# Kernel tuning notes

Measured on AMD Instinct MI355X. Metric: run time of the kernel, lower is better.

## Reference

```python
import jax, jax.numpy as jnp
import numpy as np

# --- static configuration (mirrors PMETorchPME(alpha=1.0, mesh=1.0), interpolation_nodes=6) ---
ALPHA = 1.0            # Gaussian smearing sigma of CoulombPotential
MESH_SPACING = 1.0
BOX_L = 120.0
NS = (120, 120, 120)   # ceil(BOX_L / MESH_SPACING) per axis; static for jit
ORDER = 6              # interpolation nodes (6-point stencil per axis)
N_ATOMS = 100000
PI = np.pi


def _interp_weights(x):
    # x: (N,3) offsets in [-0.5, 0.5) relative to the midpoint of the 6-point stencil.
    # Lagrange interpolation on nodes t_j = j - 2.5, j = 0..5 (even-order, midpoint-centered).
    t = np.arange(ORDER) - (ORDER - 1) / 2.0                 # (6,) node positions
    diff = x[..., None] - jnp.asarray(t, x.dtype)            # (N,3,6)
    ws = []
    for j in range(ORDER):
        idx = [k for k in range(ORDER) if k != j]
        denom = float(np.prod([t[j] - t[k] for k in idx]))
        ws.append(jnp.prod(diff[..., idx], axis=-1) / denom)
    return jnp.stack(ws, axis=-1)                            # (N,3,6)


def _stencil(coords, box):
    # Map positions to mesh units, build per-particle 6x6x6 stencil weights + flat mesh indices.
    frac = coords @ jnp.linalg.inv(box)                      # fractional coordinates
    pos = frac * jnp.asarray(NS, coords.dtype)               # (N,3) in mesh units
    i0 = jnp.floor(pos)
    x = pos - (i0 + 0.5)                                     # offset from stencil midpoint
    w = _interp_weights(x)                                   # (N,3,6)
    offs = jnp.arange(ORDER, dtype=jnp.int32) - (ORDER // 2 - 1)   # [-2..3]
    ns_i = jnp.asarray(NS, jnp.int32)
    g = (i0.astype(jnp.int32)[..., None] + offs) % ns_i[None, :, None]  # (N,3,6) periodic
    W = w[:, 0, :, None, None] * w[:, 1, None, :, None] * w[:, 2, None, None, :]   # (N,6,6,6)
    flat = (g[:, 0, :, None, None] * NS[1] + g[:, 1, None, :, None]) * NS[2] + g[:, 2, None, None, :]
    n = coords.shape[0]
    return W.reshape(n, -1), flat.reshape(n, -1)             # (N,216) each


def _kspace_kernel(box, dtype):
    # G(k) = 4*pi * exp(-sigma^2 k^2 / 2) / k^2, zero at k=0 (CoulombPotential.lr_from_k_sq)
    inv_cell = jnp.linalg.inv(box)
    m0 = jnp.fft.fftfreq(NS[0]) * NS[0]
    m1 = jnp.fft.fftfreq(NS[1]) * NS[1]
    m2 = jnp.fft.rfftfreq(NS[2]) * NS[2]
    m = jnp.stack(jnp.meshgrid(m0, m1, m2, indexing="ij"), axis=-1).astype(dtype)
    k = 2.0 * PI * jnp.einsum("xyzm,nm->xyzn", m, inv_cell)  # k = 2*pi * inv(cell) @ m
    k_sq = jnp.sum(k * k, axis=-1)
    safe = jnp.where(k_sq > 0, k_sq, 1.0)
    return jnp.where(k_sq > 0, 4.0 * PI * jnp.exp(-0.5 * ALPHA * ALPHA * k_sq) / safe, 0.0)


def setup_inputs() -> dict:
    key = jax.random.key(0)
    k1, k2 = jax.random.split(key)
    coords = jax.random.uniform(k1, (N_ATOMS, 3), dtype=jnp.float32) * BOX_L
    box = (BOX_L * jnp.eye(3, dtype=jnp.float32))
    charges = jax.random.normal(k2, (N_ATOMS, 1), dtype=jnp.float32)
    return {"coords": coords, "box": box, "charges": charges}


def reference(coords, box, charges):
    q = charges[:, 0]                                        # (N,)
    W, flat = _stencil(coords, box)                          # (N,216)
    ntot = NS[0] * NS[1] * NS[2]
    # charge spreading (scatter-add)
    mesh = jnp.zeros((ntot,), coords.dtype).at[flat.reshape(-1)].add((W * q[:, None]).reshape(-1))
    mesh = mesh.reshape(NS)
    # FFT convolution with the reciprocal-space Coulomb kernel
    G = _kspace_kernel(box, coords.dtype)
    pot_mesh = jnp.fft.irfftn(jnp.fft.rfftn(mesh, norm="backward") * G, s=NS, norm="forward")
    # gather back to particles
    pot = jnp.sum(pot_mesh.reshape(-1)[flat] * W, axis=-1)   # (N,)
    volume = jnp.abs(jnp.linalg.det(box))
    pot = pot / volume
    pot = pot - q * (np.sqrt(2.0 / PI) / ALPHA)              # remove self-contribution
    pot = pot - 2.0 * (PI * ALPHA * ALPHA) * jnp.sum(q) / volume  # charge-neutral background
    pot = pot / 2.0
    return jnp.sum(q * pot)                                  # energy = sum(charges * potentials)
```

## Files before the change

kernel.cpp:

```cpp
#include <hip/hip_runtime.h>
#include <math.h>

#define NMESH 120
#define NKZ 61
#define ALPHA_C 1.0

#define TILE 12
#define NTPD 10
#define NTILE 1000
#define FP 17
#define FPCELLS (FP*FP*FP)
#define FPSTRIDE 4928
#define CAP 256

#define CHUNK 128
#define WXA_OFF 0
#define WYA_OFF (CHUNK*17)
#define WZA_OFF (2*CHUNK*17)
#define LXS_OFF (2*CHUNK*17 + CHUNK*20)
#define SMEMF   (LXS_OFF + CHUNK)

#define YCH 12
#define XCH 4
#define YROW 137

#define NSLOT 64
#define SLOTSTRIDE 8
#define W120C (-0.052359877559829887f)

#define EK_OFF      0
#define Q_OFF       4096
#define Q2_OFF      8192
#define BUF_OFF     115264
#define C1_OFF      19827264
#define C2_OFF      115264
#define COUNTS_OFF  C1_OFF
#define SORTED_OFF  (C1_OFF + 4096)

__device__ inline void inv3(const float* b, float* ib) {
    float a00=b[0],a01=b[1],a02=b[2],a10=b[3],a11=b[4],a12=b[5],a20=b[6],a21=b[7],a22=b[8];
    float c00 =  a11*a22 - a12*a21;
    float c01 = -(a10*a22 - a12*a20);
    float c02 =  a10*a21 - a11*a20;
    float c10 = -(a01*a22 - a02*a21);
    float c11 =  a00*a22 - a02*a20;
    float c12 = -(a00*a21 - a01*a20);
    float c20 =  a01*a12 - a02*a11;
    float c21 = -(a00*a12 - a02*a10);
    float c22 =  a00*a11 - a01*a10;
    float det = a00*c00 + a01*c01 + a02*c02;
    float inv = 1.0f/det;
    ib[0]=c00*inv; ib[1]=c10*inv; ib[2]=c20*inv;
    ib[3]=c01*inv; ib[4]=c11*inv; ib[5]=c21*inv;
    ib[6]=c02*inv; ib[7]=c12*inv; ib[8]=c22*inv;
}

__device__ inline void atom_pos(const float* __restrict__ box, float c0, float c1, float c2,
                                float* p) {
    float ib[9]; inv3(box, ib);
    #pragma unroll
    for (int d=0; d<3; ++d)
        p[d] = (c0*ib[0+d] + c1*ib[3+d] + c2*ib[6+d]) * 120.0f;
}

__device__ inline int wrap120(int i) { return ((i % 120) + 120) % 120; }

__device__ inline void lag6(float x, float* w) {
    float df[6];
    #pragma unroll
    for (int k=0;k<6;++k) df[k] = x - ((float)k - 2.5f);
    w[0] = df[1]*df[2]*df[3]*df[4]*df[5] * (-1.0f/120.0f);
    w[1] = df[0]*df[2]*df[3]*df[4]*df[5] * ( 1.0f/24.0f);
    w[2] = df[0]*df[1]*df[3]*df[4]*df[5] * (-1.0f/12.0f);
    w[3] = df[0]*df[1]*df[2]*df[4]*df[5] * ( 1.0f/12.0f);
    w[4] = df[0]*df[1]*df[2]*df[3]*df[5] * (-1.0f/24.0f);
    w[5] = df[0]*df[1]*df[2]*df[3]*df[4] * ( 1.0f/120.0f);
}

__device__ inline int halo_pairs(int c, int* t, int* l) {
    int r = c % 12, ti = c / 12, n = 0;
    t[n] = ti;          l[n] = r + 2;  n++;
    if (r < 3)  { t[n] = (ti+9)%10; l[n] = r + 14; n++; }
    if (r >= 10){ t[n] = (ti+1)%10; l[n] = r - 10; n++; }
    return n;
}

__device__ inline void dft8(const float2* xin, float2* Y) {
    const float S = 0.70710678118654752f;
    float2 a=xin[0], b=xin[2], c=xin[4], d=xin[6];
    float s02r=a.x+c.x, s02i=a.y+c.y, d02r=a.x-c.x, d02i=a.y-c.y;
    float s13r=b.x+d.x, s13i=b.y+d.y, d13r=b.x-d.x, d13i=b.y-d.y;
    float2 E0 = make_float2(s02r+s13r, s02i+s13i);
    float2 E1 = make_float2(d02r+d13i, d02i-d13r);
    float2 E2 = make_float2(s02r-s13r, s02i-s13i);
    float2 E3 = make_float2(d02r-d13i, d02i+d13r);
    a=xin[1]; b=xin[3]; c=xin[5]; d=xin[7];
    s02r=a.x+c.x; s02i=a.y+c.y; d02r=a.x-c.x; d02i=a.y-c.y;
    s13r=b.x+d.x; s13i=b.y+d.y; d13r=b.x-d.x; d13i=b.y-d.y;
    float2 O0 = make_float2(s02r+s13r, s02i+s13i);
    float2 O1 = make_float2(d02r+d13i, d02i-d13r);
    float2 O2 = make_float2(s02r-s13r, s02i-s13i);
    float2 O3 = make_float2(d02r-d13i, d02i+d13r);
    float t1r = S*(O1.x + O1.y), t1i = S*(O1.y - O1.x);
    float t2r = O2.y,            t2i = -O2.x;
    float t3r = S*(O3.y - O3.x), t3i = -S*(O3.x + O3.y);
    Y[0] = make_float2(E0.x + O0.x, E0.y + O0.y);
    Y[4] = make_float2(E0.x - O0.x, E0.y - O0.y);
    Y[1] = make_float2(E1.x + t1r,  E1.y + t1i);
    Y[5] = make_float2(E1.x - t1r,  E1.y - t1i);
    Y[2] = make_float2(E2.x + t2r,  E2.y + t2i);
    Y[6] = make_float2(E2.x - t2r,  E2.y - t2i);
    Y[3] = make_float2(E3.x + t3r,  E3.y + t3i);
    Y[7] = make_float2(E3.x - t3r,  E3.y - t3i);
}

__global__ void init_kernel(int* __restrict__ counts, double* __restrict__ slots) {
    int idx = threadIdx.x;
    for (int i = idx; i < 3*NSLOT*SLOTSTRIDE; i += 1024) slots[i] = 0.0;
    for (int i = idx; i < NTILE; i += 1024) counts[i] = 0;
}

__global__ void scatter_q_kernel(const float* __restrict__ coords,
                                 const float* __restrict__ box,
                                 const float* __restrict__ charges,
                                 int* __restrict__ counts,
                                 float4* __restrict__ sorted,
                                 double* __restrict__ qslots,
                                 double* __restrict__ q2slots, int n) {
    int i = blockIdx.x*blockDim.x + threadIdx.x;
    float v = 0.f, v2 = 0.f;
    if (i < n) {
        float p[3]; atom_pos(box, coords[3*i], coords[3*i+1], coords[3*i+2], p);
        float q = charges[i];
        v = q; v2 = q*q;
        int t[3];
        #pragma unroll
        for (int d=0; d<3; ++d) t[d] = wrap120((int)floorf(p[d])) / TILE;
        int tile = (t[0]*NTPD + t[1])*NTPD + t[2];
        int idx = atomicAdd(&counts[tile], 1);
        if (idx < CAP) sorted[tile*CAP + idx] = make_float4(p[0], p[1], p[2], q);
    }
    #pragma unroll
    for (int o=32;o>0;o>>=1) { v += __shfl_down(v,o,64); v2 += __shfl_down(v2,o,64); }
    __shared__ float s1[4], s2[4];
    int lane = threadIdx.x & 63, w = threadIdx.x >> 6;
    if (lane==0) { s1[w]=v; s2[w]=v2; }
    __syncthreads();
    if (threadIdx.x==0) {
        for (int j=1;j<4;j++) { v += s1[j]; v2 += s2[j]; }
        int slot = (blockIdx.x & (NSLOT-1)) * SLOTSTRIDE;
        atomicAdd(&qslots[slot],  (double)v);
        atomicAdd(&q2slots[slot], (double)v2);
    }
}

__global__ void __launch_bounds__(320)
spread_tile_kernel(const float4* __restrict__ sorted,
                   const int* __restrict__ counts,
                   float* __restrict__ buf) {
    int tile = blockIdx.x;
    int tx = tile / (NTPD*NTPD);
    int rem = tile - tx*NTPD*NTPD;
    int ty = rem / NTPD;
    int tz = rem - ty*NTPD;
    int bx = tx*TILE, by = ty*TILE, bz = tz*TILE;

    __shared__ float smem[SMEMF];
    int* lxs = (int*)&smem[LXS_OFF];

    int tid = threadIdx.x;
    int A = tid / 17, B = tid - A*17;
    int Ac = (A > 16) ? 16 : A;
    int wv = tid >> 6, lane = tid & 63;
    int Alo = (wv*64)/17;
    int Ahi = (wv*64+63)/17; if (Ahi > 16) Ahi = 16;

    float acc[17];
    #pragma unroll
    for (int k=0;k<17;++k) acc[k] = 0.f;

    int cntT = min(counts[tile], CAP);
    const float4* src = sorted + (size_t)tile*CAP;

    for (int start = 0; start < cntT; start += CHUNK) {
        int jn = cntT - start; if (jn > CHUNK) jn = CHUNK;
        __syncthreads();
        if (tid < jn) {
            float4 s = src[start + tid];
            float fx = floorf(s.x), fy = floorf(s.y), fz = floorf(s.z);
            float wx[6]; lag6(s.x - (fx + 0.5f), wx);
            float wy[6]; lag6(s.y - (fy + 0.5f), wy);
            float wz[6]; lag6(s.z - (fz + 0.5f), wz);
            int lx = wrap120((int)fx) - bx;
            int ly = wrap120((int)fy) - by;
            int lz = wrap120((int)fz) - bz;
            #pragma unroll
            for (int k=0;k<17;++k) { smem[WXA_OFF + tid*17 + k] = 0.f;
                                     smem[WYA_OFF + tid*17 + k] = 0.f; }
            float4* wzp = (float4*)&smem[WZA_OFF + tid*20];
            float4 zz4 = make_float4(0.f,0.f,0.f,0.f);
            #pragma unroll
            for (int k=0;k<5;++k) wzp[k] = zz4;
            #pragma unroll
            for (int k=0;k<6;++k) {
                smem[WXA_OFF + tid*17 + lx + k] = wx[k];
                smem[WYA_OFF + tid*17 + ly + k] = wy[k];
                smem[WZA_OFF + tid*20 + lz + k] = wz[k]*s.w;
            }
            lxs[tid] = lx;
        }
        __syncthreads();
        int l0 = lxs[lane], l1 = lxs[64+lane];
        bool g0 = (lane < jn)    && (l0 <= Ahi) && (l0 + 5 >= Alo);
        bool g1 = (64+lane < jn) && (l1 <= Ahi) && (l1 + 5 >= Alo);
        unsigned long long m0 = __ballot(g0);
        unsigned long long m1 = __ballot(g1);
        auto body = [&](int j) {
            float wx_ = smem[WXA_OFF + j*17 + Ac];
            float wy_ = smem[WYA_OFF + j*17 + B];
            float w2 = wx_ * wy_;
            const float4* zp = (const float4*)&smem[WZA_OFF + j*20];
            float4 z0 = zp[0], z1 = zp[1], z2 = zp[2], z3 = zp[3];
            float z16 = smem[WZA_OFF + j*20 + 16];
            acc[0] = fmaf(w2,z0.x,acc[0]);  acc[1] = fmaf(w2,z0.y,acc[1]);
            acc[2] = fmaf(w2,z0.z,acc[2]);  acc[3] = fmaf(w2,z0.w,acc[3]);
            acc[4] = fmaf(w2,z1.x,acc[4]);  acc[5] = fmaf(w2,z1.y,acc[5]);
            acc[6] = fmaf(w2,z1.z,acc[6]);  acc[7] = fmaf(w2,z1.w,acc[7]);
            acc[8] = fmaf(w2,z2.x,acc[8]);  acc[9] = fmaf(w2,z2.y,acc[9]);
            acc[10]= fmaf(w2,z2.z,acc[10]); acc[11]= fmaf(w2,z2.w,acc[11]);
            acc[12]= fmaf(w2,z3.x,acc[12]); acc[13]= fmaf(w2,z3.y,acc[13]);
            acc[14]= fmaf(w2,z3.z,acc[14]); acc[15]= fmaf(w2,z3.w,acc[15]);
            acc[16]= fmaf(w2,z16, acc[16]);
        };
        while (m0) { int j = __builtin_ctzll(m0); m0 &= m0-1ull; body(j); }
        while (m1) { int j = 64 + __builtin_ctzll(m1); m1 &= m1-1ull; body(j); }
    }
    __syncthreads();
    if (tid < 289) {
        #pragma unroll
        for (int k=0;k<17;++k) smem[tid*17 + k] = acc[k];
    }
    __syncthreads();
    for (int i = tid; i < FPCELLS; i += 320)
        buf[(size_t)tile * FPSTRIDE + i] = smem[i];
}

#define DFT15_BODY(Yp, kfreq, RE, IM)                                        \
    float w1r = tw[kfreq].x, w1i = tw[kfreq].y;                              \
    float w2r = w1r*w1r - w1i*w1i, w2i = 2.f*w1r*w1i;                        \
    float w3r = w2r*w1r - w2i*w1i, w3i = w2r*w1i + w2i*w1r;                  \
    float ar=1.f, ai=0.f, br=w1r, bi=w1i, cr=w2r, ci=w2i;                    \
    float r0_=0.f,i0_=0.f,r1_=0.f,i1_=0.f,r2_=0.f,i2_=0.f;                   \
    _Pragma("unroll")                                                        \
    for (int s_=0;s_<5;++s_) {                                               \
        float2 ya = (Yp)[3*s_], yb = (Yp)[3*s_+1], yc = (Yp)[3*s_+2];        \
        r0_ = fmaf(ya.x, ar, fmaf(-ya.y, ai, r0_));                          \
        i0_ = fmaf(ya.x, ai, fmaf( ya.y, ar, i0_));                          \
        r1_ = fmaf(yb.x, br, fmaf(-yb.y, bi, r1_));                          \
        i1_ = fmaf(yb.x, bi, fmaf( yb.y, br, i1_));                          \
        r2_ = fmaf(yc.x, cr, fmaf(-yc.y, ci, r2_));                          \
        i2_ = fmaf(yc.x, ci, fmaf( yc.y, cr, i2_));                          \
        float n_;                                                            \
        n_ = ar*w3r - ai*w3i; ai = ar*w3i + ai*w3r; ar = n_;                 \
        n_ = br*w3r - bi*w3i; bi = br*w3i + bi*w3r; br = n_;                 \
        n_ = cr*w3r - ci*w3i; ci = cr*w3i + ci*w3r; cr = n_;                 \
    }                                                                        \
    float RE = (r0_+r1_)+r2_, IM = (i0_+i1_)+i2_;

#define TWIDDLE_INIT()                                                       \
    __shared__ float2 tw[120];                                               \
    for (int k_ = threadIdx.x; k_ < 120; k_ += blockDim.x) {                 \
        float s_, c_; __sincosf(W120C * (float)k_, &s_, &c_);                \
        tw[k_] = make_float2(c_, s_);                                        \
    }

__global__ void __launch_bounds__(256)
fft_z_kernel(const float* __restrict__ buf,
             float2* __restrict__ C1) {
    int x  = blockIdx.x / 10;
    int y0 = (blockIdx.x - x*10) * YCH;
    __shared__ float  lin[YCH][121];
    __shared__ float2 Ys[YCH][YROW];
    TWIDDLE_INIT()

    int txA[2], lxA[2];
    int nx = halo_pairs(x, txA, lxA);

    for (int i = threadIdx.x; i < YCH*120; i += 256) {
        int yl = i / 120, z = i - yl*120;
        int tyA[2], lyA[2]; int ny = halo_pairs(y0 + yl, tyA, lyA);
        int tzA[2], lzA[2]; int nz = halo_pairs(z, tzA, lzA);
        float s = 0.f;
        for (int ii=0; ii<nx; ++ii)
            for (int jj=0; jj<ny; ++jj)
                for (int kk=0; kk<nz; ++kk) {
                    int tile = (txA[ii]*NTPD + tyA[jj])*NTPD + tzA[kk];
                    int cell = (lxA[ii]*FP + lyA[jj])*FP + lzA[kk];
                    s += buf[(size_t)tile*FPSTRIDE + cell];
                }
        lin[yl][z] = s;
    }
    __syncthreads();
    for (int t = threadIdx.x; t < YCH*15; t += 256) {
        int yl = t / 15, j = t - (t/15)*15;
        float2 xin[8], Yo[8];
        #pragma unroll
        for (int m=0;m<8;++m) xin[m] = make_float2(lin[yl][15*m+j], 0.f);
        dft8(xin, Yo);
        #pragma unroll
        for (int r=0;r<8;++r) Ys[yl][r*17+j] = Yo[r];
    }
    __syncthreads();
    for (int o = threadIdx.x; o < YCH*NKZ; o += 256) {
        int kz = o / YCH, yl = o - (o/YCH)*YCH;
        const float2* Yp = &Ys[yl][(kz&7)*17];
        DFT15_BODY(Yp, kz, re, im)
        C1[(x*NKZ + kz)*120 + y0 + yl] = make_float2(re, im);
    }
}

__global__ void __launch_bounds__(256)
fft_y_kernel(const float2* __restrict__ C1,
             float2* __restrict__ C2) {
    int xc = blockIdx.x / NKZ;
    int kz = blockIdx.x - xc*NKZ;
    int x0 = xc * XCH;
    __shared__ float2 lin[XCH][121];
    __shared__ float2 Ys[XCH][YROW];
    TWIDDLE_INIT()
    for (int i = threadIdx.x; i < XCH*120; i += 256) {
        int xo = i / 120, y = i - (i/120)*120;
        lin[xo][y] = C1[((x0+xo)*NKZ + kz)*120 + y];
    }
    __syncthreads();
    for (int t = threadIdx.x; t < XCH*15; t += 256) {
        int xo = t / 15, j = t - (t/15)*15;
        float2 xin[8], Yo[8];
        #pragma unroll
        for (int m=0;m<8;++m) xin[m] = lin[xo][15*m+j];
        dft8(xin, Yo);
        #pragma unroll
        for (int r=0;r<8;++r) Ys[xo][r*17+j] = Yo[r];
    }
    __syncthreads();
    for (int o = threadIdx.x; o < XCH*120; o += 256) {
        int ky = o >> 2, xo = o & 3;
        const float2* Yp = &Ys[xo][(ky&7)*17];
        DFT15_BODY(Yp, ky, re, im)
        C2[(kz*120 + ky)*120 + x0 + xo] = make_float2(re, im);
    }
}

__global__ void __launch_bounds__(256)
fft_x_energy_kernel(const float2* __restrict__ C2,
                    const float* __restrict__ box,
                    double* __restrict__ ekslots) {
    int kyc = blockIdx.x / NKZ;
    int kz  = blockIdx.x - kyc*NKZ;
    int ky0 = kyc * XCH;
    __shared__ float2 lin[XCH][121];
    __shared__ float2 Ys[XCH][YROW];
    TWIDDLE_INIT()
    const float2* src = C2 + (kz*120 + ky0)*120;
    for (int i = threadIdx.x; i < XCH*120; i += 256) {
        int kyo = i / 120, xx = i - (i/120)*120;
        lin[kyo][xx] = src[i];
    }
    __syncthreads();
    for (int t = threadIdx.x; t < XCH*15; t += 256) {
        int kyo = t / 15, j = t - (t/15)*15;
        float2 xin[8], Yo[8];
        #pragma unroll
        for (int m=0;m<8;++m) xin[m] = lin[kyo][15*m+j];
        dft8(xin, Yo);
        #pragma unroll
        for (int r=0;r<8;++r) Ys[kyo][r*17+j] = Yo[r];
    }
    __syncthreads();
    float ib[9]; inv3(box, ib);
    const float TWOPI = 6.283185307179586f;
    float wzf = (kz==0 || kz==60) ? 1.0f : 2.0f;
    float contrib = 0.f;
    for (int o = threadIdx.x; o < XCH*120; o += 256) {
        int kyo = o / 120, kx = o - (o/120)*120;
        int ky = ky0 + kyo;
        const float2* Yp = &Ys[kyo][(kx&7)*17];
        DFT15_BODY(Yp, kx, re, im)
        if (!(kx==0 && ky==0 && kz==0)) {
            float mx = (kx < 60) ? (float)kx : (float)(kx - 120);
            float my = (ky < 60) ? (float)ky : (float)(ky - 120);
            float mz = (float)kz;
            float k0 = TWOPI*(mx*ib[0] + my*ib[1] + mz*ib[2]);
            float k1 = TWOPI*(mx*ib[3] + my*ib[4] + mz*ib[5]);
            float k2 = TWOPI*(mx*ib[6] + my*ib[7] + mz*ib[8]);
            float ksq = k0*k0 + k1*k1 + k2*k2;
            float G = 12.566370614359172f * __expf(-0.5f*(float)(ALPHA_C*ALPHA_C)*ksq) / ksq;
            contrib += wzf * G * (re*re + im*im);
        }
    }
    #pragma unroll
    for (int o=32;o>0;o>>=1) contrib += __shfl_down(contrib,o,64);
    __shared__ float sm[4];
    int lane = threadIdx.x & 63, w = threadIdx.x >> 6;
    if (lane==0) sm[w] = contrib;
    __syncthreads();
    if (threadIdx.x==0)
        atomicAdd(&ekslots[(blockIdx.x & (NSLOT-1)) * SLOTSTRIDE],
                  (double)(sm[0]+sm[1]+sm[2]+sm[3]));
}

__global__ void finalize_kernel(const double* __restrict__ ekslots,
                                const double* __restrict__ qslots,
                                const double* __restrict__ q2slots,
                                const float* __restrict__ box,
                                float* __restrict__ out) {
    int lane = threadIdx.x;
    double ek  = ekslots[lane*SLOTSTRIDE];
    double sq  = qslots [lane*SLOTSTRIDE];
    double sq2 = q2slots[lane*SLOTSTRIDE];
    #pragma unroll
    for (int o=32;o>0;o>>=1) {
        ek  += __shfl_down(ek,  o, 64);
        sq  += __shfl_down(sq,  o, 64);
        sq2 += __shfl_down(sq2, o, 64);
    }
    if (lane == 0) {
        double a00=box[0],a01=box[1],a02=box[2],a10=box[3],a11=box[4],a12=box[5],a20=box[6],a21=box[7],a22=box[8];
        double det = a00*(a11*a22-a12*a21) - a01*(a10*a22-a12*a20) + a02*(a10*a21-a11*a20);
        double vol = fabs(det);
        double E = ek/(2.0*vol)
                 - 0.5*sqrt(2.0/M_PI)/ALPHA_C * sq2
                 - M_PI*ALPHA_C*ALPHA_C * sq*sq / vol;
        out[0] = (float)E;
    }
}

extern "C" void kernel_launch(void* const* d_in, const int* in_sizes, int n_in,
                              void* d_out, int out_size, void* d_ws, size_t ws_size,
                              hipStream_t stream) {
    const float* coords  = (const float*)d_in[0];
    const float* box     = (const float*)d_in[1];
    const float* charges = (const float*)d_in[2];
    int n = in_sizes[0] / 3;

    char* ws = (char*)d_ws;
    double* ekslots = (double*)(ws + EK_OFF);
    double* qslots  = (double*)(ws + Q_OFF);
    double* q2slots = (double*)(ws + Q2_OFF);
    float*  buf     = (float*) (ws + BUF_OFF);
    float2* C1      = (float2*)(ws + C1_OFF);
    float2* C2      = (float2*)(ws + C2_OFF);
    int* counts     = (int*)(ws + COUNTS_OFF);
    float4* sorted  = (float4*)(ws + SORTED_OFF);

    int gA = (n + 255)/256;
    init_kernel<<<1, 1024, 0, stream>>>(counts, ekslots);
    scatter_q_kernel<<<gA, 256, 0, stream>>>(coords, box, charges, counts, sorted, qslots, q2slots, n);
    spread_tile_kernel<<<NTILE, 320, 0, stream>>>(sorted, counts, buf);
    fft_z_kernel<<<120*10, 256, 0, stream>>>(buf, C1);
    fft_y_kernel<<<30*NKZ, 256, 0, stream>>>(C1, C2);
    fft_x_energy_kernel<<<NKZ*30, 256, 0, stream>>>(C2, box, ekslots);
    finalize_kernel<<<1, 64, 0, stream>>>(ekslots, qslots, q2slots, box, (float*)d_out);
}
```

Before: 147.7 us.

## Restructure tile spreading into 128-thread blocks with packed 2-wide FMA accumulation

The spread kernel now runs 128 threads per tile. Each owner thread accumulates a column of 17 z-cells times 4 y-cells using packed float2 FMAs and float4 weight loads, instead of 289 threads each holding one (x,y) column. The footprint layout is padded to a stride of 20 in z so both the shared-memory and global writes can be float4-vectorised. The init kernel is replaced by two hipMemsetAsync calls. This aims to cut shared-memory loads per FMA, raise occupancy and speed up stores, but it adds larger per-thread register state, a bigger buffer, and a more complex skip scheme for the second wave.

```diff
diff --git a/kernel.cpp b/kernel.cpp
--- a/kernel.cpp
+++ b/kernel.cpp
@@ -9,16 +9,16 @@
 #define NTPD 10
 #define NTILE 1000
 #define FP 17
-#define FPCELLS (FP*FP*FP)
-#define FPSTRIDE 4928
+#define ZPAD 20
+#define FPSTRIDE 5792
 #define CAP 256
 
 #define CHUNK 128
 #define WXA_OFF 0
-#define WYA_OFF (CHUNK*17)
-#define WZA_OFF (2*CHUNK*17)
-#define LXS_OFF (2*CHUNK*17 + CHUNK*20)
-#define SMEMF   (LXS_OFF + CHUNK)
+#define WYA_OFF (CHUNK*ZPAD)
+#define WZA_OFF (2*CHUNK*ZPAD)
+#define LYS_OFF (3*CHUNK*ZPAD)
+#define SMEMF   (LYS_OFF + CHUNK)
 
 #define YCH 12
 #define XCH 4
@@ -27,12 +27,14 @@
 #define NSLOT 64
 #define SLOTSTRIDE 8
 #define W120C (-0.052359877559829887f)
+
+typedef float v2f __attribute__((ext_vector_type(2)));
 
 #define EK_OFF      0
 #define Q_OFF       4096
 #define Q2_OFF      8192
 #define BUF_OFF     115264
-#define C1_OFF      19827264
+#define C1_OFF      23283264
 #define C2_OFF      115264
 #define COUNTS_OFF  C1_OFF
 #define SORTED_OFF  (C1_OFF + 4096)
@@ -114,12 +116,6 @@
     Y[7] = make_float2(E3.x - t3r,  E3.y - t3i);
 }
 
-__global__ void init_kernel(int* __restrict__ counts, double* __restrict__ slots) {
-    int idx = threadIdx.x;
-    for (int i = idx; i < 3*NSLOT*SLOTSTRIDE; i += 1024) slots[i] = 0.0;
-    for (int i = idx; i < NTILE; i += 1024) counts[i] = 0;
-}
-
 __global__ void scatter_q_kernel(const float* __restrict__ coords,
                                  const float* __restrict__ box,
                                  const float* __restrict__ charges,
@@ -154,7 +150,7 @@
     }
 }
 
-__global__ void __launch_bounds__(320)
+__global__ void __launch_bounds__(128, 4)
 spread_tile_kernel(const float4* __restrict__ sorted,
                    const int* __restrict__ counts,
                    float* __restrict__ buf) {
@@ -166,18 +162,17 @@
     int bx = tx*TILE, by = ty*TILE, bz = tz*TILE;
 
     __shared__ float smem[SMEMF];
-    int* lxs = (int*)&smem[LXS_OFF];
+    int* lys = (int*)&smem[LYS_OFF];
 
     int tid = threadIdx.x;
-    int A = tid / 17, B = tid - A*17;
-    int Ac = (A > 16) ? 16 : A;
-    int wv = tid >> 6, lane = tid & 63;
-    int Alo = (wv*64)/17;
-    int Ahi = (wv*64+63)/17; if (Ahi > 16) Ahi = 16;
-
-    float acc[17];
-    #pragma unroll
-    for (int k=0;k<17;++k) acc[k] = 0.f;
+    int b = tid / 17;
+    int A = tid - b*17;
+    int bc = (b > 4) ? 4 : b;
+    bool owner = (tid < 85);
+
+    v2f acc[34];
+    #pragma unroll
+    for (int i=0;i<34;++i) acc[i] = (v2f){0.f, 0.f};
 
     int cntT = min(counts[tile], CAP);
     const float4* src = sorted + (size_t)tile*CAP;
@@ -194,55 +189,79 @@
             int lx = wrap120((int)fx) - bx;
             int ly = wrap120((int)fy) - by;
             int lz = wrap120((int)fz) - bz;
+            float4 z4 = make_float4(0.f,0.f,0.f,0.f);
+            float4* px = (float4*)&smem[WXA_OFF + tid*ZPAD];
+            float4* py = (float4*)&smem[WYA_OFF + tid*ZPAD];
+            float4* pz = (float4*)&smem[WZA_OFF + tid*ZPAD];
             #pragma unroll
-            for (int k=0;k<17;++k) { smem[WXA_OFF + tid*17 + k] = 0.f;
-                                     smem[WYA_OFF + tid*17 + k] = 0.f; }
-            float4* wzp = (float4*)&smem[WZA_OFF + tid*20];
-            float4 zz4 = make_float4(0.f,0.f,0.f,0.f);
-            #pragma unroll
-            for (int k=0;k<5;++k) wzp[k] = zz4;
+            for (int k=0;k<5;++k) { px[k]=z4; py[k]=z4; pz[k]=z4; }
             #pragma unroll
             for (int k=0;k<6;++k) {
-                smem[WXA_OFF + tid*17 + lx + k] = wx[k];
-                smem[WYA_OFF + tid*17 + ly + k] = wy[k];
-                smem[WZA_OFF + tid*20 + lz + k] = wz[k]*s.w;
+                smem[WXA_OFF + tid*ZPAD + lx + k] = wx[k];
+                smem[WYA_OFF + tid*ZPAD + ly + k] = wy[k];
+                smem[WZA_OFF + tid*ZPAD + lz + k] = wz[k]*s.w;
             }
-            lxs[tid] = lx;
+            lys[tid] = ly;
         }
         __syncthreads();
-        int l0 = lxs[lane], l1 = lxs[64+lane];
-        bool g0 = (lane < jn)    && (l0 <= Ahi) && (l0 + 5 >= Alo);
-        bool g1 = (64+lane < jn) && (l1 <= Ahi) && (l1 + 5 >= Alo);
-        unsigned long long m0 = __ballot(g0);
-        unsigned long long m1 = __ballot(g1);
         auto body = [&](int j) {
-            float wx_ = smem[WXA_OFF + j*17 + Ac];
-            float wy_ = smem[WYA_OFF + j*17 + B];
-            float w2 = wx_ * wy_;
-            const float4* zp = (const float4*)&smem[WZA_OFF + j*20];
+            float wx_ = smem[WXA_OFF + j*ZPAD + A];
+            float4 wy4 = *(const float4*)&smem[WYA_OFF + j*ZPAD + 4*bc];
+            const float4* zp = (const float4*)&smem[WZA_OFF + j*ZPAD];
             float4 z0 = zp[0], z1 = zp[1], z2 = zp[2], z3 = zp[3];
-            float z16 = smem[WZA_OFF + j*20 + 16];
-            acc[0] = fmaf(w2,z0.x,acc[0]);  acc[1] = fmaf(w2,z0.y,acc[1]);
-            acc[2] = fmaf(w2,z0.z,acc[2]);  acc[3] = fmaf(w2,z0.w,acc[3]);
-            acc[4] = fmaf(w2,z1.x,acc[4]);  acc[5] = fmaf(w2,z1.y,acc[5]);
-            acc[6] = fmaf(w2,z1.z,acc[6]);  acc[7] = fmaf(w2,z1.w,acc[7]);
-            acc[8] = fmaf(w2,z2.x,acc[8]);  acc[9] = fmaf(w2,z2.y,acc[9]);
-            acc[10]= fmaf(w2,z2.z,acc[10]); acc[11]= fmaf(w2,z2.w,acc[11]);
-            acc[12]= fmaf(w2,z3.x,acc[12]); acc[13]= fmaf(w2,z3.y,acc[13]);
-            acc[14]= fmaf(w2,z3.z,acc[14]); acc[15]= fmaf(w2,z3.w,acc[15]);
-            acc[16]= fmaf(w2,z16, acc[16]);
+            float z16 = smem[WZA_OFF + j*ZPAD + 16];
+            v2f w2a = (v2f){wx_*wy4.x, wx_*wy4.y};
+            v2f w2b = (v2f){wx_*wy4.z, wx_*wy4.w};
+            float zv[17];
+            zv[0]=z0.x;  zv[1]=z0.y;  zv[2]=z0.z;  zv[3]=z0.w;
+            zv[4]=z1.x;  zv[5]=z1.y;  zv[6]=z1.z;  zv[7]=z1.w;
+            zv[8]=z2.x;  zv[9]=z2.y;  zv[10]=z2.z; zv[11]=z2.w;
+            zv[12]=z3.x; zv[13]=z3.y; zv[14]=z3.z; zv[15]=z3.w;
+            zv[16]=z16;
+            #pragma unroll
+            for (int k=0;k<17;++k) {
+                v2f zz = (v2f){zv[k], zv[k]};
+                acc[2*k]   += w2a * zz;
+                acc[2*k+1] += w2b * zz;
+            }
         };
-        while (m0) { int j = __builtin_ctzll(m0); m0 &= m0-1ull; body(j); }
-        while (m1) { int j = 64 + __builtin_ctzll(m1); m1 &= m1-1ull; body(j); }
-    }
-    __syncthreads();
-    if (tid < 289) {
-        #pragma unroll
-        for (int k=0;k<17;++k) smem[tid*17 + k] = acc[k];
-    }
-    __syncthreads();
-    for (int i = tid; i < FPCELLS; i += 320)
-        buf[(size_t)tile * FPSTRIDE + i] = smem[i];
+        if (tid < 64) {
+            #pragma unroll 2
+            for (int j = 0; j < jn; ++j) body(j);
+        } else {
+            int lane = tid & 63;
+            int l0 = lys[lane], l1 = lys[64 + lane];
+            bool g0 = (lane < jn)      && (l0 >= 7);
+            bool g1 = (64 + lane < jn) && (l1 >= 7);
+            unsigned long long m0 = __ballot(g0);
+            unsigned long long m1 = __ballot(g1);
+            while (m0) { int j = __builtin_ctzll(m0); m0 &= m0-1ull; body(j); }
+            while (m1) { int j = 64 + __builtin_ctzll(m1); m1 &= m1-1ull; body(j); }
+        }
+    }
+    __syncthreads();
+    if (owner) {
+        #pragma unroll
+        for (int db=0; db<4; ++db) {
+            int Bv = 4*b + db;
+            if (Bv <= 16) {
+                float vals[17];
+                #pragma unroll
+                for (int k=0;k<17;++k)
+                    vals[k] = (db & 1) ? acc[2*k + (db>>1)].y : acc[2*k + (db>>1)].x;
+                float* dst = &smem[(A*17 + Bv)*ZPAD];
+                *(float4*)&dst[0]  = make_float4(vals[0], vals[1], vals[2], vals[3]);
+                *(float4*)&dst[4]  = make_float4(vals[4], vals[5], vals[6], vals[7]);
+                *(float4*)&dst[8]  = make_float4(vals[8], vals[9], vals[10],vals[11]);
+                *(float4*)&dst[12] = make_float4(vals[12],vals[13],vals[14],vals[15]);
+                dst[16] = vals[16];
+            }
+        }
+    }
+    __syncthreads();
+    float4* bp = (float4*)(buf + (size_t)tile * FPSTRIDE);
+    const float4* sp = (const float4*)smem;
+    for (int i = tid; i < FPSTRIDE/4; i += 128) bp[i] = sp[i];
 }
 
 #define DFT15_BODY(Yp, kfreq, RE, IM)                                        \
@@ -295,7 +314,7 @@
             for (int jj=0; jj<ny; ++jj)
                 for (int kk=0; kk<nz; ++kk) {
                     int tile = (txA[ii]*NTPD + tyA[jj])*NTPD + tzA[kk];
-                    int cell = (lxA[ii]*FP + lyA[jj])*FP + lzA[kk];
+                    int cell = (lxA[ii]*FP + lyA[jj])*ZPAD + lzA[kk];
                     s += buf[(size_t)tile*FPSTRIDE + cell];
                 }
         lin[yl][z] = s;
@@ -454,9 +473,10 @@
     float4* sorted  = (float4*)(ws + SORTED_OFF);
 
     int gA = (n + 255)/256;
-    init_kernel<<<1, 1024, 0, stream>>>(counts, ekslots);
+    hipMemsetAsync(ws + EK_OFF, 0, 3*4096, stream);
+    hipMemsetAsync(ws + COUNTS_OFF, 0, NTILE*sizeof(int), stream);
     scatter_q_kernel<<<gA, 256, 0, stream>>>(coords, box, charges, counts, sorted, qslots, q2slots, n);
-    spread_tile_kernel<<<NTILE, 320, 0, stream>>>(sorted, counts, buf);
+    spread_tile_kernel<<<NTILE, 128, 0, stream>>>(sorted, counts, buf);
     fft_z_kernel<<<120*10, 256, 0, stream>>>(buf, C1);
     fft_y_kernel<<<30*NKZ, 256, 0, stream>>>(C1, C2);
     fft_x_energy_kernel<<<NKZ*30, 256, 0, stream>>>(C2, box, ekslots);
```

New measurement: 153.2 us. +3.7%, slower.
